# Performance work log

Measured on AMD Instinct MI355X. Metric: run time of the kernel, lower is better.

The kernel has to match this reference:

```python
import jax, jax.numpy as jnp
import numpy as np

NUM_HEADS = 4
GROUPS = 8          # min(8, ch) with ch=256
EPS = 1e-5          # torch GroupNorm default eps


def setup_inputs() -> dict:
    key = jax.random.key(0)
    ks = jax.random.split(key, 3)
    b, c, h, w = 8, 256, 32, 32
    x = jax.random.normal(ks[0], (b, c, h, w), jnp.float32)
    gn_gamma = jnp.ones((c,), jnp.float32)
    gn_beta = jnp.zeros((c,), jnp.float32)
    qkv_w = jax.random.normal(ks[1], (3 * c, c), jnp.float32) * (c ** -0.5)
    qkv_b = jnp.zeros((3 * c,), jnp.float32)
    proj_w = jax.random.normal(ks[2], (c, c), jnp.float32) * (c ** -0.5)
    proj_b = jnp.zeros((c,), jnp.float32)
    return {"x": x, "gn_gamma": gn_gamma, "gn_beta": gn_beta,
            "qkv_w": qkv_w, "qkv_b": qkv_b, "proj_w": proj_w, "proj_b": proj_b}


def _group_norm(x, gamma, beta):
    b, c, h, w = x.shape
    xg = x.reshape(b, GROUPS, c // GROUPS, h, w)
    mean = xg.mean(axis=(2, 3, 4), keepdims=True)
    var = xg.var(axis=(2, 3, 4), keepdims=True)
    xn = ((xg - mean) * jax.lax.rsqrt(var + EPS)).reshape(b, c, h, w)
    return xn * gamma[None, :, None, None] + beta[None, :, None, None]


def reference(x, gn_gamma, gn_beta, qkv_w, qkv_b, proj_w, proj_b):
    b, c, h, w = x.shape
    dh = c // NUM_HEADS
    xn = _group_norm(x, gn_gamma, gn_beta)
    # 1x1 conv == channel matmul
    qkv = jnp.einsum('oc,bchw->bohw', qkv_w, xn) + qkv_b[None, :, None, None]
    qkv = qkv.reshape(b, 3, NUM_HEADS, dh, h * w)
    q, k, v = qkv[:, 0], qkv[:, 1], qkv[:, 2]   # each (b, n, dh, hw)
    scale = dh ** -0.5
    # full (hw x hw) attention matrix, matching the original explicit einsum
    attn = jax.nn.softmax(jnp.einsum('bncd,bnce->bnde', q, k) * scale, axis=-1)
    out = jnp.einsum('bnde,bnce->bncd', attn, v).reshape(b, c, h, w)
    out = jnp.einsum('oc,bchw->bohw', proj_w, out) + proj_b[None, :, None, None]
    return x + out
```

## Files before the change

### kernel.cpp

```cpp
#include <hip/hip_runtime.h>
#include <stdint.h>

typedef __attribute__((ext_vector_type(8))) short short8;
typedef __attribute__((ext_vector_type(4))) float f32x4;

#define BB 8
#define CC 256
#define PP 1024
#define NH 4
#define DH 64

__device__ __forceinline__ unsigned short f2bf(float f) {
  union { float f; unsigned u; } v; v.f = f;
  unsigned r = v.u + 0x7FFFu + ((v.u >> 16) & 1u);
  return (unsigned short)(r >> 16);
}

__device__ __forceinline__ f32x4 mfma16(short8 a, short8 b, f32x4 c) {
  return __builtin_amdgcn_mfma_f32_16x16x32_bf16(a, b, c, 0, 0, 0);
}

__global__ __launch_bounds__(256) void prep(
    const float* __restrict__ x, float2* __restrict__ part,
    const float* __restrict__ qkvw, const float* __restrict__ projw,
    unsigned short* __restrict__ wall) {
  int blk = blockIdx.x;
  int tid = threadIdx.x;
  if (blk < 512) {
    int sl = blk & 7, g = (blk >> 3) & 7, b = blk >> 6;
    const float4* xb =
        (const float4*)(x + (size_t)(b * CC + g * 32) * PP) + sl * 1024;
    float s = 0.f, q = 0.f;
    for (int i = tid; i < 1024; i += 256) {
      float4 v = xb[i];
      s += v.x + v.y + v.z + v.w;
      q += v.x * v.x + v.y * v.y + v.z * v.z + v.w * v.w;
    }
    for (int off = 32; off > 0; off >>= 1) {
      s += __shfl_down(s, off);
      q += __shfl_down(q, off);
    }
    __shared__ float rs[4], rq[4];
    int w = tid >> 6;
    if ((tid & 63) == 0) { rs[w] = s; rq[w] = q; }
    __syncthreads();
    if (tid == 0)
      part[blk] = make_float2(rs[0] + rs[1] + rs[2] + rs[3],
                              rq[0] + rq[1] + rq[2] + rq[3]);
  } else {
    int i4 = (blk - 512) * 256 + tid;
    float4 v = (i4 < 49152) ? ((const float4*)qkvw)[i4]
                            : ((const float4*)projw)[i4 - 49152];
    ushort4 o;
    o.x = f2bf(v.x); o.y = f2bf(v.y); o.z = f2bf(v.z); o.w = f2bf(v.w);
    ((ushort4*)wall)[i4] = o;
  }
}

__global__ __launch_bounds__(256) void norm_t(
    const float* __restrict__ x, const float2* __restrict__ part,
    const float* __restrict__ gamma, const float* __restrict__ beta,
    unsigned short* __restrict__ xnT) {
  int p0 = blockIdx.x * 64, c0 = blockIdx.y * 64, b = blockIdx.z;
  int tid = threadIdx.x;
  __shared__ float ms[2], rstd[2];
  __shared__ unsigned short T[64][72];
  if (tid < 2) {
    int g = blockIdx.y * 2 + tid;
    float S = 0.f, Q = 0.f;
    for (int i = 0; i < 8; ++i) {
      float2 pp = part[b * 64 + g * 8 + i];
      S += pp.x; Q += pp.y;
    }
    float mean = S * (1.f / 32768.f);
    float var = Q * (1.f / 32768.f) - mean * mean;
    ms[tid] = mean;
    rstd[tid] = rsqrtf(var + 1e-5f);
  }
  __syncthreads();
  for (int it = 0; it < 4; ++it) {
    int l = tid + 256 * it;
    int cc = l >> 4, p4 = l & 15;
    int c = c0 + cc, gi = cc >> 5;
    float sc = rstd[gi] * gamma[c];
    float sh = beta[c] - ms[gi] * sc;
    float4 v = *(const float4*)(x + (size_t)(b * CC + c) * PP + p0 + p4 * 4);
    T[p4 * 4 + 0][cc] = f2bf(v.x * sc + sh);
    T[p4 * 4 + 1][cc] = f2bf(v.y * sc + sh);
    T[p4 * 4 + 2][cc] = f2bf(v.z * sc + sh);
    T[p4 * 4 + 3][cc] = f2bf(v.w * sc + sh);
  }
  __syncthreads();
  for (int it = 0; it < 2; ++it) {
    int l = tid + 256 * it;
    int p = l >> 3, seg = l & 7;
    *(short8*)(xnT + ((size_t)b * PP + p0 + p) * CC + c0 + seg * 8) =
        *(const short8*)&T[p][seg * 8];
  }
}

__global__ __launch_bounds__(256) void qkv_gemm(
    const unsigned short* __restrict__ xnT, const unsigned short* __restrict__ wbf,
    const float* __restrict__ qkvb, unsigned short* __restrict__ qb,
    unsigned short* __restrict__ kb, unsigned short* __restrict__ vT) {
  int p0 = blockIdx.x * 128, o0 = blockIdx.y * 128, b = blockIdx.z;
  int tid = threadIdx.x;
  int w = tid >> 6, lane = tid & 63, lq = lane >> 4, ln = lane & 15;
  int wy = w >> 1, wx = w & 1;
  __shared__ unsigned short A_l[128][40];
  __shared__ unsigned short B_l[128][40];
  f32x4 acc[4][4];
  for (int i = 0; i < 4; ++i)
    for (int j = 0; j < 4; ++j) acc[i][j] = (f32x4){0.f, 0.f, 0.f, 0.f};
  for (int kc = 0; kc < 256; kc += 32) {
    for (int it = 0; it < 2; ++it) {
      int l = tid + 256 * it;
      int row = l >> 2, seg = l & 3;
      *(short8*)&A_l[row][seg * 8] =
          *(const short8*)(xnT + ((size_t)b * PP + p0 + row) * CC + kc + seg * 8);
      *(short8*)&B_l[row][seg * 8] =
          *(const short8*)(wbf + (size_t)(o0 + row) * CC + kc + seg * 8);
    }
    __syncthreads();
    short8 af[4], bf[4];
    for (int i = 0; i < 4; ++i)
      af[i] = *(const short8*)&A_l[wy * 64 + i * 16 + ln][lq * 8];
    for (int j = 0; j < 4; ++j)
      bf[j] = *(const short8*)&B_l[wx * 64 + j * 16 + ln][lq * 8];
    for (int i = 0; i < 4; ++i)
      for (int j = 0; j < 4; ++j) acc[i][j] = mfma16(af[i], bf[j], acc[i][j]);
    __syncthreads();
  }
  for (int i = 0; i < 4; ++i) {
    for (int j = 0; j < 4; ++j) {
      int o = o0 + wx * 64 + j * 16 + ln;
      int s = o >> 8, h = (o >> 6) & 3, ch = o & 63;
      float bias = qkvb[o];
      float mul = (s == 0) ? 0.125f : 1.0f;
      size_t bh = (size_t)b * NH + h;
      for (int r = 0; r < 4; ++r) {
        int p = p0 + wy * 64 + i * 16 + lq * 4 + r;
        unsigned short val = f2bf((acc[i][j][r] + bias) * mul);
        if (s == 2) {
          vT[(bh * DH + ch) * PP + p] = val;
        } else {
          unsigned short* dst = (s == 0) ? qb : kb;
          dst[(bh * PP + p) * DH + ch] = val;
        }
      }
    }
  }
}

__global__ __launch_bounds__(256) void attn(
    const unsigned short* __restrict__ qb, const unsigned short* __restrict__ kb,
    const unsigned short* __restrict__ vT, unsigned short* __restrict__ attnT) {
  int d0 = blockIdx.x * 64, h = blockIdx.y, b = blockIdx.z;
  int tid = threadIdx.x;
  int w = tid >> 6, lane = tid & 63, lq = lane >> 4, ln = lane & 15;
  size_t bh = (size_t)b * NH + h;
  const unsigned short* qbase = qb + bh * PP * DH;
  const unsigned short* kbase = kb + bh * PP * DH;
  const unsigned short* vbase = vT + bh * DH * PP;
  __shared__ unsigned short K_l[128][72];
  __shared__ unsigned short V_l[64][136];
  __shared__ unsigned short P_l[64][140];
  unsigned short (*O_l)[72] = (unsigned short (*)[72]) & P_l[0][0];

  int ke = tid >> 1, kseg = tid & 1;
  int vch = tid >> 2, vseg = tid & 3;

  short8 qf[2];
  {
    int d = d0 + w * 16 + ln;
    qf[0] = *(const short8*)(qbase + (size_t)d * DH + lq * 8);
    qf[1] = *(const short8*)(qbase + (size_t)d * DH + 32 + lq * 8);
  }
  float l_sum = 0.f;
  f32x4 o_acc[4];
  for (int i = 0; i < 4; ++i) o_acc[i] = (f32x4){0.f, 0.f, 0.f, 0.f};

  short8 kr[4], vr[4];
#pragma unroll
  for (int i = 0; i < 4; ++i)
    kr[i] = *(const short8*)(kbase + (size_t)ke * DH + kseg * 32 + i * 8);
#pragma unroll
  for (int i = 0; i < 4; ++i)
    vr[i] = *(const short8*)(vbase + (size_t)vch * PP + vseg * 32 + i * 8);

  for (int e0 = 0; e0 < PP; e0 += 128) {
#pragma unroll
    for (int i = 0; i < 4; ++i)
      *(short8*)&K_l[ke][kseg * 32 + i * 8] = kr[i];
#pragma unroll
    for (int i = 0; i < 4; ++i)
      *(short8*)&V_l[vch][vseg * 32 + i * 8] = vr[i];
    if (e0 + 128 < PP) {
      int en = e0 + 128;
#pragma unroll
      for (int i = 0; i < 4; ++i)
        kr[i] = *(const short8*)(kbase + (size_t)(en + ke) * DH + kseg * 32 + i * 8);
#pragma unroll
      for (int i = 0; i < 4; ++i)
        vr[i] = *(const short8*)(vbase + (size_t)vch * PP + en + vseg * 32 + i * 8);
    }
    __syncthreads();
    f32x4 sc[8];
#pragma unroll
    for (int ns = 0; ns < 8; ++ns) {
      f32x4 a = (f32x4){0.f, 0.f, 0.f, 0.f};
      a = mfma16(*(const short8*)&K_l[ns * 16 + ln][lq * 8], qf[0], a);
      a = mfma16(*(const short8*)&K_l[ns * 16 + ln][32 + lq * 8], qf[1], a);
      sc[ns] = a;
    }
#pragma unroll
    for (int ns = 0; ns < 8; ++ns) {
      float p0 = __expf(fminf(sc[ns][0], 60.f));
      float p1 = __expf(fminf(sc[ns][1], 60.f));
      float p2 = __expf(fminf(sc[ns][2], 60.f));
      float p3 = __expf(fminf(sc[ns][3], 60.f));
      l_sum += (p0 + p1) + (p2 + p3);
      union { unsigned short u[4]; unsigned long long ll; } pk;
      pk.u[0] = f2bf(p0); pk.u[1] = f2bf(p1);
      pk.u[2] = f2bf(p2); pk.u[3] = f2bf(p3);
      *(unsigned long long*)&P_l[w * 16 + ln][ns * 16 + lq * 4] = pk.ll;
    }
#pragma unroll
    for (int t = 0; t < 4; ++t) {
      short8 pb = *(const short8*)&P_l[w * 16 + ln][t * 32 + lq * 8];
#pragma unroll
      for (int cs = 0; cs < 4; ++cs)
        o_acc[cs] = mfma16(
            *(const short8*)&V_l[cs * 16 + ln][t * 32 + lq * 8], pb, o_acc[cs]);
    }
    __syncthreads();
  }
  float rsum = l_sum;
  rsum += __shfl_xor(rsum, 16);
  rsum += __shfl_xor(rsum, 32);
  float inv = 1.f / rsum;
#pragma unroll
  for (int cs = 0; cs < 4; ++cs) {
    union { unsigned short u[4]; unsigned long long ll; } pk;
#pragma unroll
    for (int r = 0; r < 4; ++r) pk.u[r] = f2bf(o_acc[cs][r] * inv);
    *(unsigned long long*)&O_l[w * 16 + ln][cs * 16 + lq * 4] = pk.ll;
  }
  __syncthreads();
  for (int it = 0; it < 2; ++it) {
    int l = tid + 256 * it;
    int dd = l >> 3, seg = l & 7;
    *(short8*)(attnT + ((size_t)b * PP + d0 + dd) * CC + h * DH + seg * 8) =
        *(const short8*)&O_l[dd][seg * 8];
  }
}

__global__ __launch_bounds__(256) void proj_gemm(
    const unsigned short* __restrict__ attnT, const unsigned short* __restrict__ pwbf,
    const float* __restrict__ projb, const float* __restrict__ x,
    float* __restrict__ out) {
  int p0 = blockIdx.x * 128, o0 = blockIdx.y * 64, b = blockIdx.z;
  int tid = threadIdx.x;
  int w = tid >> 6, lane = tid & 63, lq = lane >> 4, ln = lane & 15;
  __shared__ unsigned short A_l[64][40];
  __shared__ unsigned short B_l[128][40];
  f32x4 acc[4][2];
  for (int i = 0; i < 4; ++i)
    for (int j = 0; j < 2; ++j) acc[i][j] = (f32x4){0.f, 0.f, 0.f, 0.f};
  for (int kc = 0; kc < 256; kc += 32) {
    {
      int row = tid >> 2, seg = tid & 3;
      *(short8*)&A_l[row][seg * 8] =
          *(const short8*)(pwbf + (size_t)(o0 + row) * CC + kc + seg * 8);
    }
    for (int it = 0; it < 2; ++it) {
      int l = tid + 256 * it;
      int row = l >> 2, seg = l & 3;
      *(short8*)&B_l[row][seg * 8] =
          *(const short8*)(attnT + ((size_t)b * PP + p0 + row) * CC + kc + seg * 8);
    }
    __syncthreads();
    short8 af[4], bfr[2];
    for (int i = 0; i < 4; ++i)
      af[i] = *(const short8*)&A_l[i * 16 + ln][lq * 8];
    for (int j = 0; j < 2; ++j)
      bfr[j] = *(const short8*)&B_l[w * 32 + j * 16 + ln][lq * 8];
    for (int i = 0; i < 4; ++i)
      for (int j = 0; j < 2; ++j) acc[i][j] = mfma16(af[i], bfr[j], acc[i][j]);
    __syncthreads();
  }
  for (int i = 0; i < 4; ++i) {
    for (int j = 0; j < 2; ++j) {
      int p = p0 + w * 32 + j * 16 + ln;
      for (int r = 0; r < 4; ++r) {
        int o = o0 + i * 16 + lq * 4 + r;
        size_t idx = ((size_t)b * CC + o) * PP + p;
        out[idx] = x[idx] + projb[o] + acc[i][j][r];
      }
    }
  }
}

extern "C" void kernel_launch(void* const* d_in, const int* in_sizes, int n_in,
                              void* d_out, int out_size, void* d_ws, size_t ws_size,
                              hipStream_t stream) {
  const float* x = (const float*)d_in[0];
  const float* gamma = (const float*)d_in[1];
  const float* beta = (const float*)d_in[2];
  const float* qkvw = (const float*)d_in[3];
  const float* qkvb = (const float*)d_in[4];
  const float* projw = (const float*)d_in[5];
  const float* projb = (const float*)d_in[6];
  float* out = (float*)d_out;
  char* ws = (char*)d_ws;

  float2* part = (float2*)(ws + 0);
  unsigned short* xnT = (unsigned short*)(ws + 16384);
  unsigned short* wall = (unsigned short*)(ws + 4210688);
  unsigned short* pwbf = wall + 768 * 256;
  unsigned short* qb = (unsigned short*)(ws + 4734976);
  unsigned short* kb = (unsigned short*)(ws + 8929280);
  unsigned short* vT = (unsigned short*)(ws + 13123584);
  unsigned short* attnT = (unsigned short*)(ws + 17317888);

  prep<<<768, 256, 0, stream>>>(x, part, qkvw, projw, wall);
  norm_t<<<dim3(16, 4, 8), 256, 0, stream>>>(x, part, gamma, beta, xnT);
  qkv_gemm<<<dim3(8, 6, 8), 256, 0, stream>>>(xnT, wall, qkvb, qb, kb, vT);
  attn<<<dim3(16, 4, 8), 256, 0, stream>>>(qb, kb, vT, attnT);
  proj_gemm<<<dim3(8, 4, 8), 256, 0, stream>>>(attnT, pwbf, projb, x, out);
}
```

Baseline: 124.1 us.

## Split attention key dimension across waves with cross-wave partial-sum reduction

Each wave now takes a 32-key slice of every 128-key tile for all 64 query rows of the block, where before each wave handled 16 query rows across all keys. Every K fragment read from LDS is then reused across four query sub-tiles, which cuts LDS reads of K and V per MFMA. The cost is four times more accumulator registers per wave and a final reduction of the per-wave partial outputs and row sums through shared memory. Those partials are rounded to bf16 before they are summed, which adds rounding error.

```diff
diff --git a/kernel.cpp b/kernel.cpp
--- a/kernel.cpp
+++ b/kernel.cpp
@@ -14,6 +14,11 @@
   union { float f; unsigned u; } v; v.f = f;
   unsigned r = v.u + 0x7FFFu + ((v.u >> 16) & 1u);
   return (unsigned short)(r >> 16);
+}
+
+__device__ __forceinline__ float bf2f(unsigned short u) {
+  union { unsigned u; float f; } v; v.u = ((unsigned)u) << 16;
+  return v.f;
 }
 
 __device__ __forceinline__ f32x4 mfma16(short8 a, short8 b, f32x4 c) {
@@ -162,23 +167,31 @@
   const unsigned short* qbase = qb + bh * PP * DH;
   const unsigned short* kbase = kb + bh * PP * DH;
   const unsigned short* vbase = vT + bh * DH * PP;
-  __shared__ unsigned short K_l[128][72];
-  __shared__ unsigned short V_l[64][136];
-  __shared__ unsigned short P_l[64][140];
-  unsigned short (*O_l)[72] = (unsigned short (*)[72]) & P_l[0][0];
+
+  __shared__ __align__(16) char SM[53248];
+  unsigned short (*K_l)[72] = (unsigned short (*)[72])(SM);
+  unsigned short (*V_l)[136] = (unsigned short (*)[136])(SM + 18432);
+  unsigned short (*P_l)[136] = (unsigned short (*)[136])(SM + 35840);
+  unsigned short* Obf = (unsigned short*)(SM);
+  float* lsums = (float*)(SM + 36864);
 
   int ke = tid >> 1, kseg = tid & 1;
   int vch = tid >> 2, vseg = tid & 3;
 
-  short8 qf[2];
-  {
-    int d = d0 + w * 16 + ln;
-    qf[0] = *(const short8*)(qbase + (size_t)d * DH + lq * 8);
-    qf[1] = *(const short8*)(qbase + (size_t)d * DH + 32 + lq * 8);
-  }
-  float l_sum = 0.f;
-  f32x4 o_acc[4];
-  for (int i = 0; i < 4; ++i) o_acc[i] = (f32x4){0.f, 0.f, 0.f, 0.f};
+  short8 qf[4][2];
+#pragma unroll
+  for (int ds = 0; ds < 4; ++ds)
+#pragma unroll
+    for (int kc = 0; kc < 2; ++kc)
+      qf[ds][kc] = *(const short8*)(qbase + (size_t)(d0 + ds * 16 + ln) * DH +
+                                    kc * 32 + lq * 8);
+
+  float lsum[4] = {0.f, 0.f, 0.f, 0.f};
+  f32x4 o_acc[4][4];
+#pragma unroll
+  for (int i = 0; i < 4; ++i)
+#pragma unroll
+    for (int j = 0; j < 4; ++j) o_acc[i][j] = (f32x4){0.f, 0.f, 0.f, 0.f};
 
   short8 kr[4], vr[4];
 #pragma unroll
@@ -205,53 +218,88 @@
         vr[i] = *(const short8*)(vbase + (size_t)vch * PP + en + vseg * 32 + i * 8);
     }
     __syncthreads();
-    f32x4 sc[8];
-#pragma unroll
-    for (int ns = 0; ns < 8; ++ns) {
-      f32x4 a = (f32x4){0.f, 0.f, 0.f, 0.f};
-      a = mfma16(*(const short8*)&K_l[ns * 16 + ln][lq * 8], qf[0], a);
-      a = mfma16(*(const short8*)&K_l[ns * 16 + ln][32 + lq * 8], qf[1], a);
-      sc[ns] = a;
-    }
-#pragma unroll
-    for (int ns = 0; ns < 8; ++ns) {
-      float p0 = __expf(fminf(sc[ns][0], 60.f));
-      float p1 = __expf(fminf(sc[ns][1], 60.f));
-      float p2 = __expf(fminf(sc[ns][2], 60.f));
-      float p3 = __expf(fminf(sc[ns][3], 60.f));
-      l_sum += (p0 + p1) + (p2 + p3);
+#pragma unroll
+    for (int es = 0; es < 2; ++es) {
+      short8 ka0 = *(const short8*)&K_l[w * 32 + es * 16 + ln][lq * 8];
+      short8 ka1 = *(const short8*)&K_l[w * 32 + es * 16 + ln][32 + lq * 8];
+      f32x4 sc[4];
+#pragma unroll
+      for (int ds = 0; ds < 4; ++ds) {
+        f32x4 a = (f32x4){0.f, 0.f, 0.f, 0.f};
+        a = mfma16(ka0, qf[ds][0], a);
+        a = mfma16(ka1, qf[ds][1], a);
+        sc[ds] = a;
+      }
+#pragma unroll
+      for (int ds = 0; ds < 4; ++ds) {
+        float p0 = __expf(fminf(sc[ds][0], 60.f));
+        float p1 = __expf(fminf(sc[ds][1], 60.f));
+        float p2 = __expf(fminf(sc[ds][2], 60.f));
+        float p3 = __expf(fminf(sc[ds][3], 60.f));
+        lsum[ds] += (p0 + p1) + (p2 + p3);
+        union { unsigned short u[4]; unsigned long long ll; } pk;
+        pk.u[0] = f2bf(p0); pk.u[1] = f2bf(p1);
+        pk.u[2] = f2bf(p2); pk.u[3] = f2bf(p3);
+        *(unsigned long long*)&P_l[ds * 16 + ln][w * 32 + es * 16 + lq * 4] =
+            pk.ll;
+      }
+    }
+    short8 pb[4];
+#pragma unroll
+    for (int ds = 0; ds < 4; ++ds)
+      pb[ds] = *(const short8*)&P_l[ds * 16 + ln][w * 32 + lq * 8];
+#pragma unroll
+    for (int cs = 0; cs < 4; ++cs) {
+      short8 va = *(const short8*)&V_l[cs * 16 + ln][w * 32 + lq * 8];
+#pragma unroll
+      for (int ds = 0; ds < 4; ++ds)
+        o_acc[cs][ds] = mfma16(va, pb[ds], o_acc[cs][ds]);
+    }
+    __syncthreads();
+  }
+#pragma unroll
+  for (int ds = 0; ds < 4; ++ds) {
+    float s = lsum[ds];
+    s += __shfl_xor(s, 16);
+    s += __shfl_xor(s, 32);
+    if (lq == 0) lsums[w * 64 + ds * 16 + ln] = s;
+  }
+#pragma unroll
+  for (int cs = 0; cs < 4; ++cs) {
+#pragma unroll
+    for (int ds = 0; ds < 4; ++ds) {
       union { unsigned short u[4]; unsigned long long ll; } pk;
-      pk.u[0] = f2bf(p0); pk.u[1] = f2bf(p1);
-      pk.u[2] = f2bf(p2); pk.u[3] = f2bf(p3);
-      *(unsigned long long*)&P_l[w * 16 + ln][ns * 16 + lq * 4] = pk.ll;
-    }
-#pragma unroll
-    for (int t = 0; t < 4; ++t) {
-      short8 pb = *(const short8*)&P_l[w * 16 + ln][t * 32 + lq * 8];
-#pragma unroll
-      for (int cs = 0; cs < 4; ++cs)
-        o_acc[cs] = mfma16(
-            *(const short8*)&V_l[cs * 16 + ln][t * 32 + lq * 8], pb, o_acc[cs]);
-    }
-    __syncthreads();
-  }
-  float rsum = l_sum;
-  rsum += __shfl_xor(rsum, 16);
-  rsum += __shfl_xor(rsum, 32);
-  float inv = 1.f / rsum;
-#pragma unroll
-  for (int cs = 0; cs < 4; ++cs) {
-    union { unsigned short u[4]; unsigned long long ll; } pk;
-#pragma unroll
-    for (int r = 0; r < 4; ++r) pk.u[r] = f2bf(o_acc[cs][r] * inv);
-    *(unsigned long long*)&O_l[w * 16 + ln][cs * 16 + lq * 4] = pk.ll;
+#pragma unroll
+      for (int r = 0; r < 4; ++r) pk.u[r] = f2bf(o_acc[cs][ds][r]);
+      *(unsigned long long*)&Obf[((w * 64 + ds * 16 + ln) * 72) + cs * 16 +
+                                 lq * 4] = pk.ll;
+    }
   }
   __syncthreads();
-  for (int it = 0; it < 2; ++it) {
-    int l = tid + 256 * it;
-    int dd = l >> 3, seg = l & 7;
-    *(short8*)(attnT + ((size_t)b * PP + d0 + dd) * CC + h * DH + seg * 8) =
-        *(const short8*)&O_l[dd][seg * 8];
+  {
+    int d = tid >> 2, cr = tid & 3;
+    float inv = 1.f / (lsums[d] + lsums[64 + d] + lsums[128 + d] + lsums[192 + d]);
+    float o[16];
+#pragma unroll
+    for (int j = 0; j < 16; ++j) o[j] = 0.f;
+#pragma unroll
+    for (int ww = 0; ww < 4; ++ww) {
+#pragma unroll
+      for (int jj = 0; jj < 4; ++jj) {
+        unsigned long long v = *(const unsigned long long*)&Obf[
+            ((ww * 64 + d) * 72) + cr * 16 + jj * 4];
+#pragma unroll
+        for (int r = 0; r < 4; ++r)
+          o[jj * 4 + r] += bf2f((unsigned short)(v >> (16 * r)));
+      }
+    }
+    union { unsigned short u[16]; short8 s[2]; } pk;
+#pragma unroll
+    for (int j = 0; j < 16; ++j) pk.u[j] = f2bf(o[j] * inv);
+    unsigned short* dst =
+        attnT + ((size_t)b * PP + d0 + d) * CC + h * DH + cr * 16;
+    *(short8*)dst = pk.s[0];
+    *(short8*)(dst + 8) = pk.s[1];
   }
 }
 
```

New measurement: 125.3 us. Within noise of the previous version (+1.0%).

## Split attention key range across warps, halve query tile, use exp2 softmax

Applied to the files above, without the earlier changes.

The attention kernel now gives each block 32 queries instead of 64 and splits each 64-key tile between warp pairs. This doubles the grid to 1024 blocks and shrinks shared memory, so occupancy rises. Partial outputs and row sums from the two key halves are combined through shared memory (as bf16) at the end. The Q scale now folds in log2(e) so exp2f can replace __expf. In exchange, K/V tiles are reloaded twice as often across blocks, each tile step runs fewer MFMAs per barrier, and the bf16 partial sums add rounding.

```diff
diff --git a/kernel.cpp b/kernel.cpp
--- a/kernel.cpp
+++ b/kernel.cpp
@@ -14,6 +14,11 @@
   union { float f; unsigned u; } v; v.f = f;
   unsigned r = v.u + 0x7FFFu + ((v.u >> 16) & 1u);
   return (unsigned short)(r >> 16);
+}
+
+__device__ __forceinline__ float bf2f(unsigned short u) {
+  union { unsigned u; float f; } v; v.u = ((unsigned)u) << 16;
+  return v.f;
 }
 
 __device__ __forceinline__ f32x4 mfma16(short8 a, short8 b, f32x4 c) {
@@ -136,7 +141,7 @@
       int o = o0 + wx * 64 + j * 16 + ln;
       int s = o >> 8, h = (o >> 6) & 3, ch = o & 63;
       float bias = qkvb[o];
-      float mul = (s == 0) ? 0.125f : 1.0f;
+      float mul = (s == 0) ? 0.18033688011112042f : 1.0f;
       size_t bh = (size_t)b * NH + h;
       for (int r = 0; r < 4; ++r) {
         int p = p0 + wy * 64 + i * 16 + lq * 4 + r;
@@ -155,103 +160,118 @@
 __global__ __launch_bounds__(256) void attn(
     const unsigned short* __restrict__ qb, const unsigned short* __restrict__ kb,
     const unsigned short* __restrict__ vT, unsigned short* __restrict__ attnT) {
-  int d0 = blockIdx.x * 64, h = blockIdx.y, b = blockIdx.z;
+  int d0 = blockIdx.x * 32, h = blockIdx.y, b = blockIdx.z;
   int tid = threadIdx.x;
   int w = tid >> 6, lane = tid & 63, lq = lane >> 4, ln = lane & 15;
+  int dw = w & 1, ew = w >> 1;
   size_t bh = (size_t)b * NH + h;
   const unsigned short* qbase = qb + bh * PP * DH;
   const unsigned short* kbase = kb + bh * PP * DH;
   const unsigned short* vbase = vT + bh * DH * PP;
-  __shared__ unsigned short K_l[128][72];
-  __shared__ unsigned short V_l[64][136];
-  __shared__ unsigned short P_l[64][140];
-  unsigned short (*O_l)[72] = (unsigned short (*)[72]) & P_l[0][0];
-
-  int ke = tid >> 1, kseg = tid & 1;
-  int vch = tid >> 2, vseg = tid & 3;
+
+  __shared__ __align__(16) char SM[23552];
+  unsigned short (*K_l)[72] = (unsigned short (*)[72])(SM);
+  unsigned short (*V_l)[72] = (unsigned short (*)[72])(SM + 9216);
+  unsigned short* Pw = (unsigned short*)(SM + 18432) + w * 640;
+  unsigned short (*Obf)[72] = (unsigned short (*)[72])(SM);
+  float* lsums = (float*)(SM + 9216);
+
+  int srow = tid >> 2, sseg = tid & 3;
 
   short8 qf[2];
   {
-    int d = d0 + w * 16 + ln;
+    int d = d0 + dw * 16 + ln;
     qf[0] = *(const short8*)(qbase + (size_t)d * DH + lq * 8);
     qf[1] = *(const short8*)(qbase + (size_t)d * DH + 32 + lq * 8);
   }
-  float l_sum = 0.f;
+  float lsum = 0.f;
   f32x4 o_acc[4];
   for (int i = 0; i < 4; ++i) o_acc[i] = (f32x4){0.f, 0.f, 0.f, 0.f};
 
-  short8 kr[4], vr[4];
-#pragma unroll
-  for (int i = 0; i < 4; ++i)
-    kr[i] = *(const short8*)(kbase + (size_t)ke * DH + kseg * 32 + i * 8);
-#pragma unroll
-  for (int i = 0; i < 4; ++i)
-    vr[i] = *(const short8*)(vbase + (size_t)vch * PP + vseg * 32 + i * 8);
-
-  for (int e0 = 0; e0 < PP; e0 += 128) {
-#pragma unroll
-    for (int i = 0; i < 4; ++i)
-      *(short8*)&K_l[ke][kseg * 32 + i * 8] = kr[i];
-#pragma unroll
-    for (int i = 0; i < 4; ++i)
-      *(short8*)&V_l[vch][vseg * 32 + i * 8] = vr[i];
-    if (e0 + 128 < PP) {
-      int en = e0 + 128;
-#pragma unroll
-      for (int i = 0; i < 4; ++i)
-        kr[i] = *(const short8*)(kbase + (size_t)(en + ke) * DH + kseg * 32 + i * 8);
-#pragma unroll
-      for (int i = 0; i < 4; ++i)
-        vr[i] = *(const short8*)(vbase + (size_t)vch * PP + en + vseg * 32 + i * 8);
-    }
-    __syncthreads();
-    f32x4 sc[8];
-#pragma unroll
-    for (int ns = 0; ns < 8; ++ns) {
+  short8 kr[2], vr[2];
+#pragma unroll
+  for (int i = 0; i < 2; ++i) {
+    kr[i] = *(const short8*)(kbase + (size_t)srow * DH + sseg * 16 + i * 8);
+    vr[i] = *(const short8*)(vbase + (size_t)srow * PP + sseg * 16 + i * 8);
+  }
+
+  for (int e0 = 0; e0 < PP; e0 += 64) {
+#pragma unroll
+    for (int i = 0; i < 2; ++i) {
+      *(short8*)&K_l[srow][sseg * 16 + i * 8] = kr[i];
+      *(short8*)&V_l[srow][sseg * 16 + i * 8] = vr[i];
+    }
+    if (e0 + 64 < PP) {
+      int en = e0 + 64;
+#pragma unroll
+      for (int i = 0; i < 2; ++i) {
+        kr[i] = *(const short8*)(kbase + (size_t)(en + srow) * DH + sseg * 16 + i * 8);
+        vr[i] = *(const short8*)(vbase + (size_t)srow * PP + en + sseg * 16 + i * 8);
+      }
+    }
+    __syncthreads();
+    f32x4 sc[2];
+#pragma unroll
+    for (int es = 0; es < 2; ++es) {
+      int er = ew * 32 + es * 16 + ln;
       f32x4 a = (f32x4){0.f, 0.f, 0.f, 0.f};
-      a = mfma16(*(const short8*)&K_l[ns * 16 + ln][lq * 8], qf[0], a);
-      a = mfma16(*(const short8*)&K_l[ns * 16 + ln][32 + lq * 8], qf[1], a);
-      sc[ns] = a;
-    }
-#pragma unroll
-    for (int ns = 0; ns < 8; ++ns) {
-      float p0 = __expf(fminf(sc[ns][0], 60.f));
-      float p1 = __expf(fminf(sc[ns][1], 60.f));
-      float p2 = __expf(fminf(sc[ns][2], 60.f));
-      float p3 = __expf(fminf(sc[ns][3], 60.f));
-      l_sum += (p0 + p1) + (p2 + p3);
+      a = mfma16(*(const short8*)&K_l[er][lq * 8], qf[0], a);
+      a = mfma16(*(const short8*)&K_l[er][32 + lq * 8], qf[1], a);
+      sc[es] = a;
+    }
+#pragma unroll
+    for (int es = 0; es < 2; ++es) {
+      float p0 = exp2f(fminf(sc[es][0], 86.f));
+      float p1 = exp2f(fminf(sc[es][1], 86.f));
+      float p2 = exp2f(fminf(sc[es][2], 86.f));
+      float p3 = exp2f(fminf(sc[es][3], 86.f));
+      lsum += (p0 + p1) + (p2 + p3);
       union { unsigned short u[4]; unsigned long long ll; } pk;
       pk.u[0] = f2bf(p0); pk.u[1] = f2bf(p1);
       pk.u[2] = f2bf(p2); pk.u[3] = f2bf(p3);
-      *(unsigned long long*)&P_l[w * 16 + ln][ns * 16 + lq * 4] = pk.ll;
-    }
-#pragma unroll
-    for (int t = 0; t < 4; ++t) {
-      short8 pb = *(const short8*)&P_l[w * 16 + ln][t * 32 + lq * 8];
-#pragma unroll
-      for (int cs = 0; cs < 4; ++cs)
-        o_acc[cs] = mfma16(
-            *(const short8*)&V_l[cs * 16 + ln][t * 32 + lq * 8], pb, o_acc[cs]);
-    }
-    __syncthreads();
-  }
-  float rsum = l_sum;
-  rsum += __shfl_xor(rsum, 16);
-  rsum += __shfl_xor(rsum, 32);
-  float inv = 1.f / rsum;
+      *(unsigned long long*)&Pw[ln * 40 + es * 16 + lq * 4] = pk.ll;
+    }
+    short8 pb = *(const short8*)&Pw[ln * 40 + lq * 8];
+#pragma unroll
+    for (int cs = 0; cs < 4; ++cs) {
+      short8 va = *(const short8*)&V_l[cs * 16 + ln][ew * 32 + lq * 8];
+      o_acc[cs] = mfma16(va, pb, o_acc[cs]);
+    }
+    __syncthreads();
+  }
+  {
+    float s = lsum;
+    s += __shfl_xor(s, 16);
+    s += __shfl_xor(s, 32);
+    if (lq == 0) lsums[w * 16 + ln] = s;
+  }
 #pragma unroll
   for (int cs = 0; cs < 4; ++cs) {
     union { unsigned short u[4]; unsigned long long ll; } pk;
 #pragma unroll
-    for (int r = 0; r < 4; ++r) pk.u[r] = f2bf(o_acc[cs][r] * inv);
-    *(unsigned long long*)&O_l[w * 16 + ln][cs * 16 + lq * 4] = pk.ll;
+    for (int r = 0; r < 4; ++r) pk.u[r] = f2bf(o_acc[cs][r]);
+    *(unsigned long long*)&Obf[w * 16 + ln][cs * 16 + lq * 4] = pk.ll;
   }
   __syncthreads();
-  for (int it = 0; it < 2; ++it) {
-    int l = tid + 256 * it;
-    int dd = l >> 3, seg = l & 7;
-    *(short8*)(attnT + ((size_t)b * PP + d0 + dd) * CC + h * DH + seg * 8) =
-        *(const short8*)&O_l[dd][seg * 8];
+  {
+    int d = tid >> 3, cseg = tid & 7;
+    int dl = d & 15, dh2 = d >> 4;
+    float inv =
+        1.f / (lsums[dh2 * 16 + dl] + lsums[(2 + dh2) * 16 + dl]);
+    float o[8];
+#pragma unroll
+    for (int j = 0; j < 8; ++j) o[j] = 0.f;
+#pragma unroll
+    for (int ewp = 0; ewp < 2; ++ewp) {
+      short8 vv = *(const short8*)&Obf[(ewp * 2 + dh2) * 16 + dl][cseg * 8];
+#pragma unroll
+      for (int j = 0; j < 8; ++j) o[j] += bf2f((unsigned short)vv[j]);
+    }
+    union { unsigned short u[8]; short8 s; } pk;
+#pragma unroll
+    for (int j = 0; j < 8; ++j) pk.u[j] = f2bf(o[j] * inv);
+    *(short8*)(attnT + ((size_t)b * PP + d0 + d) * CC + h * DH + cseg * 8) =
+        pk.s;
   }
 }
 
@@ -326,6 +346,6 @@
   prep<<<768, 256, 0, stream>>>(x, part, qkvw, projw, wall);
   norm_t<<<dim3(16, 4, 8), 256, 0, stream>>>(x, part, gamma, beta, xnT);
   qkv_gemm<<<dim3(8, 6, 8), 256, 0, stream>>>(xnT, wall, qkvb, qb, kb, vT);
-  attn<<<dim3(16, 4, 8), 256, 0, stream>>>(qb, kb, vT, attnT);
+  attn<<<dim3(32, 4, 8), 256, 0, stream>>>(qb, kb, vT, attnT);
   proj_gemm<<<dim3(8, 4, 8), 256, 0, stream>>>(attnT, pwbf, projb, x, out);
 }
```

Measured after the change: 126.0 us. No clear change (+1.6%).
